# Kernel tuning notes

Hardware: AMD Instinct MI355X
Metric: run time of the kernel (lower is better)

Reference implementation:

```python
import jax, jax.numpy as jnp
import numpy as np

B, L, V, DIN, H = 256, 256, 2048, 128, 256   # trees, leaves/tree, vocab, in_dim, mem_dim
NODES = 2 * L - 1                            # perfect binary tree, level-by-level layout
LEVELS = int(np.log2(L)) + 1                 # 9 levels: 256,128,...,1 nodes


def setup_inputs() -> dict:
    key = jax.random.key(0)
    ks = jax.random.split(key, 32)
    w = lambda k, shape: jax.random.normal(k, shape, jnp.float32) * 0.05
    inp = {
        "input_ids": jax.random.randint(ks[0], (B, NODES), 0, V),
        "emb": w(ks[1], (V, DIN)),
        # iou projections (i,o,u concatenated -> 3H)
        "Wioux": w(ks[2], (DIN, 3 * H)), "bioux": jnp.zeros((3 * H,), jnp.float32),
        "Wiouh1": w(ks[3], (H, 3 * H)), "biouh1": jnp.zeros((3 * H,), jnp.float32),
        "Wiouh2": w(ks[4], (H, 3 * H)), "biouh2": jnp.zeros((3 * H,), jnp.float32),
        # forget gates
        "Wfx": w(ks[5], (DIN, H)), "bfx": jnp.zeros((H,), jnp.float32),
        "Wfh11": w(ks[6], (H, H)), "bfh11": jnp.zeros((H,), jnp.float32),
        "Wfh12": w(ks[7], (H, H)), "bfh12": jnp.zeros((H,), jnp.float32),
        "Wfh21": w(ks[8], (H, H)), "bfh21": jnp.zeros((H,), jnp.float32),
        "Wfh22": w(ks[9], (H, H)), "bfh22": jnp.zeros((H,), jnp.float32),
        # classifier head
        "Wl1": w(ks[10], (H, 100)), "bl1": jnp.zeros((100,), jnp.float32),
        "Wl2": w(ks[11], (100, 1)), "bl2": jnp.zeros((1,), jnp.float32),
    }
    return inp


def reference(input_ids, emb, Wioux, bioux, Wiouh1, biouh1, Wiouh2, biouh2,
              Wfx, bfx, Wfh11, bfh11, Wfh12, bfh12, Wfh21, bfh21, Wfh22, bfh22,
              Wl1, bl1, Wl2, bl2):
    emb = emb.at[0].set(0.0)                 # padding_idx=0
    xemb = emb[input_ids]                    # [B, NODES, DIN]

    def cell(x, h1, h2, c1, c2):
        iou = (x @ Wioux + bioux) + (h1 @ Wiouh1 + biouh1) + (h2 @ Wiouh2 + biouh2)
        i, o, u = jnp.split(iou, 3, axis=-1)
        i, o, u = jax.nn.sigmoid(i), jax.nn.sigmoid(o), jnp.tanh(u)
        fx = x @ Wfx + bfx
        f0 = jax.nn.sigmoid((h1 @ Wfh11 + bfh11) + (h2 @ Wfh12 + bfh12) + fx)
        f1 = jax.nn.sigmoid((h1 @ Wfh21 + bfh21) + (h2 @ Wfh22 + bfh22) + fx)
        c = i * u + f0 * c1 + f1 * c2
        h = o * jnp.tanh(c)
        return h, c

    # leaves: zero child states
    z = jnp.zeros((B, L, H), jnp.float32)
    h, c = cell(xemb[:, :L], z, z, z, z)     # [B, L, H]

    off, n = 0, L
    for _ in range(LEVELS - 1):              # fixed small structural loop (8 iters)
        off += n
        n //= 2
        x = xemb[:, off:off + n]             # [B, n, DIN]
        h, c = cell(x, h[:, 0::2], h[:, 1::2], c[:, 0::2], c[:, 1::2])

    root_h = h[:, 0]                         # [B, H]
    hid = root_h @ Wl1 + bl1                 # linear1
    pred = (jax.nn.relu(hid) @ Wl2 + bl2)[..., 0]   # [B], arithmetic head (no softmax)
    return pred
```

## Files before the change

kernel.cpp:

```cpp
#include <hip/hip_runtime.h>
#include <math.h>

#define B_ 256
#define L_ 256
#define V_ 2048
#define DIN_ 128
#define H_ 256
#define NODES_ 511

typedef _Float16 half8 __attribute__((ext_vector_type(8)));
typedef float f32x4 __attribute__((ext_vector_type(4)));

__device__ __forceinline__ float sigm(float x) { return 1.f / (1.f + __expf(-x)); }
__device__ __forceinline__ float tanh_f(float x) {
    float xc = fminf(fmaxf(x, -15.f), 15.f);
    float e = __expf(2.f * xc);
    return (e - 1.f) / (e + 1.f);
}
__device__ __forceinline__ void gload16(const void* g, void* l) {
    __builtin_amdgcn_global_load_lds((const __attribute__((address_space(1))) unsigned int*)g,
                                     (__attribute__((address_space(3))) unsigned int*)l, 16, 0, 0);
}

__global__ void build_WTh(_Float16* __restrict__ WTh,
    const float* __restrict__ Wiouh1, const float* __restrict__ Wfh11, const float* __restrict__ Wfh21,
    const float* __restrict__ Wiouh2, const float* __restrict__ Wfh12, const float* __restrict__ Wfh22)
{
    int e = blockIdx.x * 256 + threadIdx.x;
    int nn = e >> 9, k = e & 511;
    int g = nn >> 8, t = nn & 255;
    float v;
    if (k < 256) {
        v = (g < 3) ? Wiouh1[k * 768 + nn] : ((g == 3) ? Wfh11[k * 256 + t] : Wfh21[k * 256 + t]);
    } else {
        int kp = k - 256;
        v = (g < 3) ? Wiouh2[kp * 768 + nn] : ((g == 3) ? Wfh12[kp * 256 + t] : Wfh22[kp * 256 + t]);
    }
    WTh[e] = (_Float16)v;
}

__global__ __launch_bounds__(256) void build_table(float* __restrict__ tab, const float* __restrict__ emb,
    const float* __restrict__ Wioux, const float* __restrict__ Wfx,
    const float* __restrict__ bioux, const float* __restrict__ biouh1, const float* __restrict__ biouh2,
    const float* __restrict__ bfx, const float* __restrict__ bfh11, const float* __restrict__ bfh12,
    const float* __restrict__ bfh21, const float* __restrict__ bfh22)
{
    __shared__ float As[64][33];
    __shared__ float Ws[32][65];
    const int tid = threadIdx.x, tx = tid & 15, ty = tid >> 4;
    const int i0 = blockIdx.x * 64, c0 = blockIdx.y * 64;
    const int g = c0 >> 8;
    float acc[4][4];
    #pragma unroll
    for (int i = 0; i < 4; ++i)
        #pragma unroll
        for (int j = 0; j < 4; ++j) acc[i][j] = 0.f;

    for (int k0 = 0; k0 < 128; k0 += 32) {
        #pragma unroll
        for (int it = 0; it < 2; ++it) {
            int f = tid + it * 256;
            int row = f >> 3, kk = (f & 7) * 4;
            int gr = i0 + row;
            float4 av = (gr == 0) ? make_float4(0.f, 0.f, 0.f, 0.f)
                                  : *(const float4*)(emb + (size_t)gr * 128 + k0 + kk);
            As[row][kk] = av.x; As[row][kk + 1] = av.y; As[row][kk + 2] = av.z; As[row][kk + 3] = av.w;
            int k = f >> 4, cc = (f & 15) * 4;
            int col = c0 + cc;
            float4 wv = (g < 3) ? *(const float4*)(Wioux + (size_t)(k0 + k) * 768 + col)
                                : *(const float4*)(Wfx + (size_t)(k0 + k) * 256 + (col & 255));
            Ws[k][cc] = wv.x; Ws[k][cc + 1] = wv.y; Ws[k][cc + 2] = wv.z; Ws[k][cc + 3] = wv.w;
        }
        __syncthreads();
        #pragma unroll 8
        for (int k = 0; k < 32; ++k) {
            float a[4], w[4];
            #pragma unroll
            for (int i = 0; i < 4; ++i) a[i] = As[ty * 4 + i][k];
            #pragma unroll
            for (int j = 0; j < 4; ++j) w[j] = Ws[k][tx * 4 + j];
            #pragma unroll
            for (int i = 0; i < 4; ++i)
                #pragma unroll
                for (int j = 0; j < 4; ++j) acc[i][j] = fmaf(a[i], w[j], acc[i][j]);
        }
        __syncthreads();
    }
    #pragma unroll
    for (int j = 0; j < 4; ++j) {
        int col = c0 + tx * 4 + j; int t = col & 255;
        float bs = (g < 3) ? (bioux[col] + biouh1[col] + biouh2[col])
                 : (g == 3) ? (bfx[t] + bfh11[t] + bfh12[t])
                            : (bfx[t] + bfh21[t] + bfh22[t]);
        #pragma unroll
        for (int i = 0; i < 4; ++i)
            tab[(size_t)(i0 + ty * 4 + i) * 1280 + col] = acc[i][j] + bs;
    }
}

__global__ void build_h0c0(const float* __restrict__ tab, _Float16* __restrict__ H0h, float* __restrict__ H0c) {
    int id = blockIdx.x, t = threadIdx.x;
    const float* tp = tab + (size_t)id * 1280 + t;
    float vi = sigm(tp[0]), vo = sigm(tp[256]), vu = tanh_f(tp[512]);
    float c = vi * vu;
    H0h[id * 256 + t] = (_Float16)(vo * tanh_f(c));
    H0c[id * 256 + t] = c;
}

template<bool LVL1, int RT>
__global__ __launch_bounds__(256, 2) void cell5(
    const _Float16* __restrict__ WTh, const float* __restrict__ tab,
    const int* __restrict__ ids,
    const _Float16* __restrict__ h_prev, const float* __restrict__ c_prev,
    _Float16* __restrict__ h_out, float* __restrict__ c_out,
    int n, int ln, int off)
{
    constexpr int BM = RT * 64;
    __shared__ _Float16 Bs[80 * 256];
    const int tid = threadIdx.x, lane = tid & 63, wid = tid >> 6;
    const int l15 = lane & 15, lg = lane >> 4;
    const int rowB = blockIdx.x * BM;
    const int t0 = blockIdx.y * 16;

    const _Float16* aPA[RT];
    const _Float16* aPB[RT];
    #pragma unroll
    for (int rt = 0; rt < RT; ++rt) {
        int row = rowB + wid * (RT * 16) + rt * 16 + l15;
        if constexpr (LVL1) {
            int b = row >> 7, j = row & 127;
            aPA[rt] = h_prev + (size_t)ids[b * NODES_ + 2 * j] * 256 + lg * 8;
            aPB[rt] = h_prev + (size_t)ids[b * NODES_ + 2 * j + 1] * 256 + lg * 8;
        } else {
            aPA[rt] = h_prev + (size_t)row * 512 + lg * 8;
            aPB[rt] = aPA[rt] + 256;
        }
    }

    const _Float16* sp[10];
    #pragma unroll
    for (int i = 0; i < 10; ++i) {
        int slot = tid + i * 256;
        int nr = slot >> 5, j = slot & 31;
        int g = nr >> 4, tl = nr & 15;
        sp[i] = WTh + (size_t)(g * 256 + t0 + tl) * 512 + ((j ^ (nr & 7)) * 8);
    }
    #pragma unroll
    for (int i = 0; i < 10; ++i)
        gload16(sp[i], &Bs[(size_t)(tid + i * 256) * 8]);
    half8 breg[10];
    #pragma unroll
    for (int i = 0; i < 10; ++i) breg[i] = *(const half8*)(sp[i] + 256);

    half8 aF[2][RT];
    #pragma unroll
    for (int rt = 0; rt < RT; ++rt) aF[0][rt] = *(const half8*)(aPA[rt]);

    f32x4 acc[RT][5];
    #pragma unroll
    for (int rt = 0; rt < RT; ++rt)
        #pragma unroll
        for (int g = 0; g < 5; ++g) acc[rt][g] = (f32x4)0.f;

    __syncthreads();

    #pragma unroll
    for (int s = 0; s < 8; ++s) {
        const int cur = s & 1, nxt = cur ^ 1;
        #pragma unroll
        for (int rt = 0; rt < RT; ++rt)
            aF[nxt][rt] = (s < 7) ? *(const half8*)(aPA[rt] + (s + 1) * 32)
                                  : *(const half8*)(aPB[rt]);
        #pragma unroll
        for (int g = 0; g < 5; ++g) {
            int nr = g * 16 + l15;
            int j = (s * 4 + lg) ^ (nr & 7);
            half8 bF = *(const half8*)&Bs[(size_t)(nr * 32 + j) * 8];
            #pragma unroll
            for (int rt = 0; rt < RT; ++rt)
                acc[rt][g] = __builtin_amdgcn_mfma_f32_16x16x32_f16(aF[cur][rt], bF, acc[rt][g], 0, 0, 0);
        }
    }

    __syncthreads();
    #pragma unroll
    for (int i = 0; i < 10; ++i)
        *(half8*)&Bs[(size_t)(tid + i * 256) * 8] = breg[i];
    __syncthreads();

    #pragma unroll
    for (int s = 0; s < 8; ++s) {
        const int cur = s & 1, nxt = cur ^ 1;
        if (s < 7) {
            #pragma unroll
            for (int rt = 0; rt < RT; ++rt)
                aF[nxt][rt] = *(const half8*)(aPB[rt] + (s + 1) * 32);
        }
        #pragma unroll
        for (int g = 0; g < 5; ++g) {
            int nr = g * 16 + l15;
            int j = (s * 4 + lg) ^ (nr & 7);
            half8 bF = *(const half8*)&Bs[(size_t)(nr * 32 + j) * 8];
            #pragma unroll
            for (int rt = 0; rt < RT; ++rt)
                acc[rt][g] = __builtin_amdgcn_mfma_f32_16x16x32_f16(aF[cur][rt], bF, acc[rt][g], 0, 0, 0);
        }
    }

    const int tcol = t0 + l15;
    #pragma unroll
    for (int rt = 0; rt < RT; ++rt) {
        #pragma unroll
        for (int q = 0; q < 4; ++q) {
            int row = rowB + wid * (RT * 16) + rt * 16 + lg * 4 + q;
            int b = row >> ln, j = row & (n - 1);
            int id = ids[b * NODES_ + off + j];
            const float* tp = tab + (size_t)id * 1280 + tcol;
            float c1, c2;
            if constexpr (LVL1) {
                int bb = row >> 7, jj = row & 127;
                c1 = c_prev[(size_t)ids[bb * NODES_ + 2 * jj] * 256 + tcol];
                c2 = c_prev[(size_t)ids[bb * NODES_ + 2 * jj + 1] * 256 + tcol];
            } else {
                const float* cpp = c_prev + (size_t)row * 512 + tcol;
                c1 = cpp[0]; c2 = cpp[256];
            }
            float vi  = sigm(acc[rt][0][q] + tp[0]);
            float vo  = sigm(acc[rt][1][q] + tp[256]);
            float vu  = tanh_f(acc[rt][2][q] + tp[512]);
            float vf0 = sigm(acc[rt][3][q] + tp[768]);
            float vf1 = sigm(acc[rt][4][q] + tp[1024]);
            float c = vi * vu + vf0 * c1 + vf1 * c2;
            size_t ob = (size_t)row * 256 + tcol;
            h_out[ob] = (_Float16)(vo * tanh_f(c));
            c_out[ob] = c;
        }
    }
}

__global__ void head_kernel(const _Float16* __restrict__ hroot,
    const float* __restrict__ Wl1, const float* __restrict__ bl1,
    const float* __restrict__ Wl2, const float* __restrict__ bl2,
    float* __restrict__ out)
{
    __shared__ float hrow[H_];
    __shared__ float red[256];
    int b = blockIdx.x; int tid = threadIdx.x;
    hrow[tid] = (float)hroot[(size_t)b * H_ + tid];
    __syncthreads();
    float v = 0.f;
    if (tid < 100) {
        float s = bl1[tid];
        for (int k = 0; k < H_; ++k) s = fmaf(hrow[k], Wl1[k * 100 + tid], s);
        v = fmaxf(s, 0.f) * Wl2[tid];
    }
    red[tid] = v;
    __syncthreads();
    for (int s = 128; s > 0; s >>= 1) { if (tid < s) red[tid] += red[tid + s]; __syncthreads(); }
    if (tid == 0) out[b] = red[0] + bl2[0];
}

extern "C" void kernel_launch(void* const* d_in, const int* in_sizes, int n_in,
                              void* d_out, int out_size, void* d_ws, size_t ws_size,
                              hipStream_t stream) {
    const int*   ids    = (const int*)d_in[0];
    const float* emb    = (const float*)d_in[1];
    const float* Wioux  = (const float*)d_in[2];
    const float* bioux  = (const float*)d_in[3];
    const float* Wiouh1 = (const float*)d_in[4];
    const float* biouh1 = (const float*)d_in[5];
    const float* Wiouh2 = (const float*)d_in[6];
    const float* biouh2 = (const float*)d_in[7];
    const float* Wfx    = (const float*)d_in[8];
    const float* bfx    = (const float*)d_in[9];
    const float* Wfh11  = (const float*)d_in[10];
    const float* bfh11  = (const float*)d_in[11];
    const float* Wfh12  = (const float*)d_in[12];
    const float* bfh12  = (const float*)d_in[13];
    const float* Wfh21  = (const float*)d_in[14];
    const float* bfh21  = (const float*)d_in[15];
    const float* Wfh22  = (const float*)d_in[16];
    const float* bfh22  = (const float*)d_in[17];
    const float* Wl1    = (const float*)d_in[18];
    const float* bl1    = (const float*)d_in[19];
    const float* Wl2    = (const float*)d_in[20];
    const float* bl2    = (const float*)d_in[21];
    float* out = (float*)d_out;

    char* wsb = (char*)d_ws;
    _Float16* WTh = (_Float16*)(wsb);
    float*    tab = (float*)(wsb + 1310720);
    _Float16* H0h = (_Float16*)(wsb + 11796480);
    float*    H0c = (float*)(wsb + 12845056);
    _Float16* hA  = (_Float16*)(wsb + 14942208);
    _Float16* hB  = (_Float16*)(wsb + 23330816);
    float*    cA  = (float*)(wsb + 40108032);
    float*    cB  = (float*)(wsb + 56885248);

    build_WTh<<<dim3(2560), 256, 0, stream>>>(WTh, Wiouh1, Wfh11, Wfh21, Wiouh2, Wfh12, Wfh22);
    build_table<<<dim3(32, 20), 256, 0, stream>>>(tab, emb, Wioux, Wfx,
        bioux, biouh1, biouh2, bfx, bfh11, bfh12, bfh21, bfh22);
    build_h0c0<<<dim3(2048), 256, 0, stream>>>(tab, H0h, H0c);

    cell5<true, 4><<<dim3(128, 16), 256, 0, stream>>>(WTh, tab, ids, H0h, H0c, hB, cB, 128, 7, 256);

    _Float16 *hp = hB, *hn = hA;
    float    *cp = cB, *cn = cA;
    int off = 384, n = 64, ln = 6;
    for (int lvl = 2; lvl <= 8; ++lvl) {
        int M = B_ * n;
        if (M >= 4096)
            cell5<false, 4><<<dim3(M / 256, 16), 256, 0, stream>>>(WTh, tab, ids, hp, cp, hn, cn, n, ln, off);
        else
            cell5<false, 1><<<dim3(M / 64, 16), 256, 0, stream>>>(WTh, tab, ids, hp, cp, hn, cn, n, ln, off);
        off += n; n >>= 1; --ln;
        _Float16* t1 = hp; hp = hn; hn = t1;
        float*    t2 = cp; cp = cn; cn = t2;
    }

    head_kernel<<<dim3(256), 256, 0, stream>>>(hp, Wl1, bl1, Wl2, bl2, out);
}
```

Before: 293.2 us.

## Restage second weight half via async LDS loads, deepen A prefetch, retune tiles

The second half of the weight tile is no longer staged through registers. It is reloaded straight into LDS with async global-to-LDS loads after the first half's MFMA loop, which frees the ten half8 breg registers. The A-fragment prefetch moves from double to triple buffering, loading two steps ahead. Launch bounds go from 2 to 3 blocks per SM, and the small-level path switches from RT=1 to RT=2 with the RT=4 threshold raised to M>=8192. The intent is more occupancy and better latency hiding, at the cost of a second exposed weight load between the two K halves.

```diff
diff --git a/kernel.cpp b/kernel.cpp
--- a/kernel.cpp
+++ b/kernel.cpp
@@ -107,8 +107,20 @@
     H0c[id * 256 + t] = c;
 }
 
+__device__ __forceinline__ void stageB(const _Float16* __restrict__ WTh, _Float16* Bs,
+                                       int tid, int t0, int kof) {
+    #pragma unroll
+    for (int i = 0; i < 10; ++i) {
+        int f = tid + i * 256;
+        int n = f >> 5, j = f & 31;
+        int ng = (n >> 4) * 256 + t0 + (n & 15);
+        const _Float16* src = WTh + (size_t)ng * 512 + kof + ((j ^ (n & 7)) * 8);
+        gload16(src, &Bs[(size_t)f * 8]);
+    }
+}
+
 template<bool LVL1, int RT>
-__global__ __launch_bounds__(256, 2) void cell5(
+__global__ __launch_bounds__(256, 3) void cell6(
     const _Float16* __restrict__ WTh, const float* __restrict__ tab,
     const int* __restrict__ ids,
     const _Float16* __restrict__ h_prev, const float* __restrict__ c_prev,
@@ -116,7 +128,7 @@
     int n, int ln, int off)
 {
     constexpr int BM = RT * 64;
-    __shared__ _Float16 Bs[80 * 256];
+    __shared__ _Float16 Bs[80 * 32 * 8];
     const int tid = threadIdx.x, lane = tid & 63, wid = tid >> 6;
     const int l15 = lane & 15, lg = lane >> 4;
     const int rowB = blockIdx.x * BM;
@@ -137,40 +149,29 @@
         }
     }
 
-    const _Float16* sp[10];
-    #pragma unroll
-    for (int i = 0; i < 10; ++i) {
-        int slot = tid + i * 256;
-        int nr = slot >> 5, j = slot & 31;
-        int g = nr >> 4, tl = nr & 15;
-        sp[i] = WTh + (size_t)(g * 256 + t0 + tl) * 512 + ((j ^ (nr & 7)) * 8);
-    }
-    #pragma unroll
-    for (int i = 0; i < 10; ++i)
-        gload16(sp[i], &Bs[(size_t)(tid + i * 256) * 8]);
-    half8 breg[10];
-    #pragma unroll
-    for (int i = 0; i < 10; ++i) breg[i] = *(const half8*)(sp[i] + 256);
-
-    half8 aF[2][RT];
+    stageB(WTh, Bs, tid, t0, 0);
+
+    f32x4 acc[RT][5];
+    #pragma unroll
+    for (int rt = 0; rt < RT; ++rt)
+        #pragma unroll
+        for (int g = 0; g < 5; ++g) acc[rt][g] = (f32x4)0.f;
+
+    half8 aF[3][RT];
     #pragma unroll
     for (int rt = 0; rt < RT; ++rt) aF[0][rt] = *(const half8*)(aPA[rt]);
-
-    f32x4 acc[RT][5];
-    #pragma unroll
-    for (int rt = 0; rt < RT; ++rt)
-        #pragma unroll
-        for (int g = 0; g < 5; ++g) acc[rt][g] = (f32x4)0.f;
+    #pragma unroll
+    for (int rt = 0; rt < RT; ++rt) aF[1][rt] = *(const half8*)(aPA[rt] + 32);
 
     __syncthreads();
 
     #pragma unroll
     for (int s = 0; s < 8; ++s) {
-        const int cur = s & 1, nxt = cur ^ 1;
+        const int pf = s + 2;
         #pragma unroll
         for (int rt = 0; rt < RT; ++rt)
-            aF[nxt][rt] = (s < 7) ? *(const half8*)(aPA[rt] + (s + 1) * 32)
-                                  : *(const half8*)(aPB[rt]);
+            aF[pf % 3][rt] = (pf < 8) ? *(const half8*)(aPA[rt] + pf * 32)
+                                      : *(const half8*)(aPB[rt] + (pf - 8) * 32);
         #pragma unroll
         for (int g = 0; g < 5; ++g) {
             int nr = g * 16 + l15;
@@ -178,32 +179,30 @@
             half8 bF = *(const half8*)&Bs[(size_t)(nr * 32 + j) * 8];
             #pragma unroll
             for (int rt = 0; rt < RT; ++rt)
-                acc[rt][g] = __builtin_amdgcn_mfma_f32_16x16x32_f16(aF[cur][rt], bF, acc[rt][g], 0, 0, 0);
-        }
-    }
-
-    __syncthreads();
-    #pragma unroll
-    for (int i = 0; i < 10; ++i)
-        *(half8*)&Bs[(size_t)(tid + i * 256) * 8] = breg[i];
-    __syncthreads();
-
-    #pragma unroll
-    for (int s = 0; s < 8; ++s) {
-        const int cur = s & 1, nxt = cur ^ 1;
-        if (s < 7) {
+                acc[rt][g] = __builtin_amdgcn_mfma_f32_16x16x32_f16(aF[s % 3][rt], bF, acc[rt][g], 0, 0, 0);
+        }
+    }
+
+    __syncthreads();
+    stageB(WTh, Bs, tid, t0, 256);
+    __syncthreads();
+
+    #pragma unroll
+    for (int s = 8; s < 16; ++s) {
+        const int pf = s + 2;
+        if (pf < 16) {
             #pragma unroll
             for (int rt = 0; rt < RT; ++rt)
-                aF[nxt][rt] = *(const half8*)(aPB[rt] + (s + 1) * 32);
+                aF[pf % 3][rt] = *(const half8*)(aPB[rt] + (pf - 8) * 32);
         }
         #pragma unroll
         for (int g = 0; g < 5; ++g) {
             int nr = g * 16 + l15;
-            int j = (s * 4 + lg) ^ (nr & 7);
+            int j = ((s & 7) * 4 + lg) ^ (nr & 7);
             half8 bF = *(const half8*)&Bs[(size_t)(nr * 32 + j) * 8];
             #pragma unroll
             for (int rt = 0; rt < RT; ++rt)
-                acc[rt][g] = __builtin_amdgcn_mfma_f32_16x16x32_f16(aF[cur][rt], bF, acc[rt][g], 0, 0, 0);
+                acc[rt][g] = __builtin_amdgcn_mfma_f32_16x16x32_f16(aF[s % 3][rt], bF, acc[rt][g], 0, 0, 0);
         }
     }
 
@@ -302,17 +301,17 @@
         bioux, biouh1, biouh2, bfx, bfh11, bfh12, bfh21, bfh22);
     build_h0c0<<<dim3(2048), 256, 0, stream>>>(tab, H0h, H0c);
 
-    cell5<true, 4><<<dim3(128, 16), 256, 0, stream>>>(WTh, tab, ids, H0h, H0c, hB, cB, 128, 7, 256);
+    cell6<true, 4><<<dim3(128, 16), 256, 0, stream>>>(WTh, tab, ids, H0h, H0c, hB, cB, 128, 7, 256);
 
     _Float16 *hp = hB, *hn = hA;
     float    *cp = cB, *cn = cA;
     int off = 384, n = 64, ln = 6;
     for (int lvl = 2; lvl <= 8; ++lvl) {
         int M = B_ * n;
-        if (M >= 4096)
-            cell5<false, 4><<<dim3(M / 256, 16), 256, 0, stream>>>(WTh, tab, ids, hp, cp, hn, cn, n, ln, off);
+        if (M >= 8192)
+            cell6<false, 4><<<dim3(M / 256, 16), 256, 0, stream>>>(WTh, tab, ids, hp, cp, hn, cn, n, ln, off);
         else
-            cell5<false, 1><<<dim3(M / 64, 16), 256, 0, stream>>>(WTh, tab, ids, hp, cp, hn, cn, n, ln, off);
+            cell6<false, 2><<<dim3(M / 128, 16), 256, 0, stream>>>(WTh, tab, ids, hp, cp, hn, cn, n, ln, off);
         off += n; n >>= 1; --ln;
         _Float16* t1 = hp; hp = hn; hn = t1;
         float*    t2 = cp; cp = cn; cn = t2;
```

New measurement: 296.7 us. Within noise of the previous version (+1.2%).
